# Kernel optimization log

Measured on AMD Instinct MI355X. Metric: run time of the kernel, lower is better.

Reference implementation:

```python
import jax, jax.numpy as jnp
import numpy as np

N = 100000   # nodes
E = 600000   # edges
D = 128      # input = hidden = output dim
L = 3        # GNN layers
C = 40       # num_classes
EPS = 1e-5   # BatchNorm eps


def setup_inputs() -> dict:
    key = jax.random.key(0)
    ks = jax.random.split(key, 8)
    x = jax.random.normal(ks[0], (N, D), jnp.float32)
    edge_index = jax.random.randint(ks[1], (2, E), 0, N, jnp.int32)
    # GCNConv weights per layer (Glorot-ish scale), bias zeros
    Ws = jax.random.normal(ks[2], (L, D, D), jnp.float32) / np.sqrt(D)
    bs = jnp.zeros((L, D), jnp.float32)
    # BatchNorm affine params
    gammas = jnp.ones((L, D), jnp.float32)
    betas = jnp.zeros((L, D), jnp.float32)
    # PReLU single slope per layer (torch default init 0.25)
    prelu_a = jnp.full((L,), 0.25, jnp.float32)
    # classification head: Linear(D,D) -> ReLU -> Linear(D,C)
    Wh1 = jax.random.normal(ks[3], (D, D), jnp.float32) / np.sqrt(D)
    bh1 = jnp.zeros((D,), jnp.float32)
    Wh2 = jax.random.normal(ks[4], (D, C), jnp.float32) / np.sqrt(D)
    bh2 = jnp.zeros((C,), jnp.float32)
    return dict(x=x, edge_index=edge_index, Ws=Ws, bs=bs, gammas=gammas,
                betas=betas, prelu_a=prelu_a, Wh1=Wh1, bh1=bh1, Wh2=Wh2, bh2=bh2)


def _gcn_conv(h, src, dst, norm, W, b):
    # PyG GCNConv: out_i = sum_{j->i} norm_ij * (x_j W) + b  (self-loops already in src/dst)
    m = (h @ W)[src] * norm[:, None]          # [E+N, D_out]
    return jax.ops.segment_sum(m, dst, num_segments=N) + b


def reference(x, edge_index, Ws, bs, gammas, betas, prelu_a, Wh1, bh1, Wh2, bh2):
    # add self-loops + symmetric normalization (computed once; same graph each layer)
    loops = jnp.arange(N, dtype=edge_index.dtype)
    src = jnp.concatenate([edge_index[0], loops])
    dst = jnp.concatenate([edge_index[1], loops])
    deg = jax.ops.segment_sum(jnp.ones_like(dst, jnp.float32), dst, num_segments=N)
    dinv = jax.lax.rsqrt(jnp.maximum(deg, 1.0))  # deg >= 1 thanks to self-loops
    norm = dinv[src] * dinv[dst]                 # [E+N]

    h = x
    for l in range(L):
        h = _gcn_conv(h, src, dst, norm, Ws[l], bs[l])
        # BatchNorm in training mode: batch statistics over nodes
        mu = h.mean(axis=0)
        var = h.var(axis=0)
        h = (h - mu) * jax.lax.rsqrt(var + EPS) * gammas[l] + betas[l]
        # PReLU
        h = jnp.where(h > 0, h, prelu_a[l] * h)

    embeddings = h
    logits = jax.nn.relu(embeddings @ Wh1 + bh1) @ Wh2 + bh2
    out = jnp.argmax(logits, axis=1)
    return embeddings, logits, out
```

## Files before the change

### kernel.cpp

```cpp
#include <hip/hip_runtime.h>
#include <hip/hip_bf16.h>
#include <cstddef>

#define N_NODES 100000
#define N_EDGES 600000
#define DD 128
#define LL 3
#define CC 40
#define BN_EPS 1e-5f

typedef __attribute__((ext_vector_type(8))) short bfrag;
typedef __attribute__((ext_vector_type(4))) float f32x4;

__device__ __forceinline__ float ldf(const void* p, long i, int f32) {
    return f32 ? ((const float*)p)[i] : __bfloat162float(((const __hip_bfloat16*)p)[i]);
}
__device__ __forceinline__ void stf(void* p, long i, float v, int f32) {
    if (f32) ((float*)p)[i] = v;
    else     ((__hip_bfloat16*)p)[i] = __float2bfloat16(v);
}

__device__ __forceinline__ unsigned short f2bf(float f) {
    unsigned u = __float_as_uint(f);
    unsigned r = (u + 0x7fffu + ((u >> 16) & 1u)) >> 16;
    return (unsigned short)r;
}
__device__ __forceinline__ float bf2f(unsigned short h) {
    return __uint_as_float(((unsigned)h) << 16);
}

__global__ __launch_bounds__(256) void k_detect(const void* __restrict__ x, int* __restrict__ dflag) {
    __shared__ int s[256];
    int t = threadIdx.x;
    const __hip_bfloat16* xb = (const __hip_bfloat16*)x;
    int bad = 0;
    for (int i = t; i < 4096; i += 256) {
        float v = __bfloat162float(xb[i]);
        float a = fabsf(v);
        if (!(a < 1e6f)) bad++;
        else if (v != 0.f && a < 1e-30f) bad++;
    }
    s[t] = bad; __syncthreads();
    for (int off = 128; off > 0; off >>= 1) {
        if (t < off) s[t] += s[t + off];
        __syncthreads();
    }
    if (t == 0) *dflag = (s[0] > 64) ? 1 : 0;
}

__global__ __launch_bounds__(256) void k_packw(const void* __restrict__ Ws, const void* __restrict__ Wh1,
                                               unsigned short* __restrict__ Wp,
                                               const int* __restrict__ dflag) {
    int f = *dflag;
    int u = blockIdx.x * 256 + threadIdx.x;
    int mat = u >> 14;
    int r = u & 16383;
    int k = r >> 7, c = r & 127;
    float wv = (mat < 3) ? ldf(Ws, (long)mat * 16384 + r, f) : ldf(Wh1, r, f);
    unsigned short hi = f2bf(wv);
    float r1 = wv - bf2f(hi);
    unsigned short mid = f2bf(r1);
    float r2 = r1 - bf2f(mid);
    unsigned short lo = f2bf(r2);
    int n = c >> 4, ks = k >> 5, j = k & 7;
    int lanep = (c & 15) | (((k >> 3) & 3) << 4);
    long base = (long)mat * 49152 + (long)((n * 4 + ks) * 3) * 512 + lanep * 8 + j;
    Wp[base] = hi;
    Wp[base + 512] = mid;
    Wp[base + 1024] = lo;
}


__global__ __launch_bounds__(256) void k_init(int* cnt, int* fpos, int* rowptr, float* stats) {
    int i = blockIdx.x * 256 + threadIdx.x;
    if (i < N_NODES) { cnt[i] = 0; fpos[i] = 0; }
    if (i < 6 * DD) stats[i] = 0.f;
    if (i == 0) rowptr[N_NODES] = N_EDGES;
}

__global__ __launch_bounds__(256) void k_count(const int* __restrict__ ei, int* __restrict__ cnt) {
    int e = blockIdx.x * 256 + threadIdx.x;
    if (e < N_EDGES) atomicAdd(&cnt[ei[N_EDGES + e]], 1);
}

__global__ __launch_bounds__(256) void k_scan1(const int* __restrict__ cnt, int* __restrict__ rowptr,
                                               int* __restrict__ bsum, float* __restrict__ dinv) {
    __shared__ int s[256];
    int t = threadIdx.x;
    int i = blockIdx.x * 256 + t;
    int v = (i < N_NODES) ? cnt[i] : 0;
    if (i < N_NODES) dinv[i] = 1.f / sqrtf((float)(1 + v));
    s[t] = v; __syncthreads();
    for (int off = 1; off < 256; off <<= 1) {
        int x = (t >= off) ? s[t - off] : 0;
        __syncthreads();
        s[t] += x; __syncthreads();
    }
    if (i < N_NODES) rowptr[i] = s[t] - v;
    if (t == 255) bsum[blockIdx.x] = s[255];
}

__global__ __launch_bounds__(512) void k_scan2(int* bsum, int nb) {
    __shared__ int s[512];
    int t = threadIdx.x;
    int v = (t < nb) ? bsum[t] : 0;
    s[t] = v; __syncthreads();
    for (int off = 1; off < 512; off <<= 1) {
        int x = (t >= off) ? s[t - off] : 0;
        __syncthreads();
        s[t] += x; __syncthreads();
    }
    if (t < nb) bsum[t] = s[t] - v;
}

__global__ __launch_bounds__(256) void k_scan3(int* rowptr, const int* __restrict__ bsum) {
    int i = blockIdx.x * 256 + threadIdx.x;
    if (i < N_NODES) rowptr[i] += bsum[blockIdx.x];
}

__global__ __launch_bounds__(256) void k_fill(const int* __restrict__ ei, int* __restrict__ fpos,
                                              const int* __restrict__ rowptr, int* __restrict__ adj) {
    int e = blockIdx.x * 256 + threadIdx.x;
    if (e < N_EDGES) {
        int d = ei[N_EDGES + e];
        int p = atomicAdd(&fpos[d], 1);
        adj[rowptr[d] + p] = ei[e];
    }
}

__device__ __forceinline__ void load_act(const void* __restrict__ src, long row, int lane, int f,
                                         const float* __restrict__ bnp,
                                         float s0, float s1, float h0, float h1, float al,
                                         float& o0, float& o1) {
    if (bnp) {
        float2 v = ((const float2*)src)[row * 64 + lane];
        float y0 = fmaf(v.x, s0, h0), y1 = fmaf(v.y, s1, h1);
        o0 = (y0 > 0.f) ? y0 : al * y0;
        o1 = (y1 > 0.f) ? y1 : al * y1;
    } else if (f) {
        float2 v = ((const float2*)src)[row * 64 + lane];
        o0 = v.x; o1 = v.y;
    } else {
        unsigned u = ((const unsigned*)src)[row * 64 + lane];
        o0 = __uint_as_float(u << 16);
        o1 = __uint_as_float(u & 0xffff0000u);
    }
}


__global__ __launch_bounds__(256) void k_agg(const void* __restrict__ src,
                                             const int* __restrict__ rowptr,
                                             const int* __restrict__ adj,
                                             const float* __restrict__ dinv,
                                             const float* __restrict__ bnp,
                                             float* __restrict__ outp,
                                             const int* __restrict__ dflag) {
    int f = *dflag;
    int lane = threadIdx.x & 63;
    int i = blockIdx.x * 4 + (threadIdx.x >> 6);
    if (i >= N_NODES) return;
    float s0 = 0.f, s1 = 0.f, h0 = 0.f, h1 = 0.f, al = 0.f;
    if (bnp) {
        s0 = bnp[2 * lane];       s1 = bnp[2 * lane + 1];
        h0 = bnp[128 + 2 * lane]; h1 = bnp[129 + 2 * lane];
        al = bnp[256];
    }
    float di = dinv[i];
    int e0 = rowptr[i], e1 = rowptr[i + 1];
    float x0, x1;
    load_act(src, i, lane, f, bnp, s0, s1, h0, h1, al, x0, x1);
    float acc0 = di * x0, acc1 = di * x1;

    for (int base = e0; base < e1; base += 64) {
        int m = e1 - base; if (m > 64) m = 64;
        int aj = (lane < m) ? adj[base + lane] : 0;
        float djl = (lane < m) ? dinv[aj] : 0.f;
        int t = 0;
        for (; t + 2 <= m; t += 2) {
            int j0 = __shfl(aj, t), j1 = __shfl(aj, t + 1);
            float d0 = __shfl(djl, t), d1 = __shfl(djl, t + 1);
            float p0, p1, q0, q1;
            load_act(src, j0, lane, f, bnp, s0, s1, h0, h1, al, p0, p1);
            load_act(src, j1, lane, f, bnp, s0, s1, h0, h1, al, q0, q1);
            acc0 += d0 * p0 + d1 * q0;
            acc1 += d0 * p1 + d1 * q1;
        }
        if (t < m) {
            int j0 = __shfl(aj, t);
            float d0 = __shfl(djl, t);
            float p0, p1;
            load_act(src, j0, lane, f, bnp, s0, s1, h0, h1, al, p0, p1);
            acc0 += d0 * p0;
            acc1 += d0 * p1;
        }
    }
    float2 r; r.x = di * acc0; r.y = di * acc1;
    ((float2*)outp)[(size_t)i * 64 + lane] = r;
}


__global__ __launch_bounds__(256, 2) void k_gemm2(const float* __restrict__ A,
                                                  const unsigned short* __restrict__ Wp,
                                                  const void* __restrict__ bias, long boff,
                                                  const float* __restrict__ bnpA,
                                                  float* __restrict__ stats,
                                                  float* __restrict__ Cout, int relu,
                                                  const int* __restrict__ dflag) {
    __shared__ unsigned short Wl[24576];
    int f = *dflag;
    int tid = threadIdx.x;

    int lane = tid & 63;
    int w = tid >> 6;
    int lr = lane & 15;
    int lg = lane >> 4;
    int rowbase = blockIdx.x * 128 + w * 32;

    float bcol[8];
    #pragma unroll
    for (int n = 0; n < 8; ++n)
        bcol[n] = bias ? ldf(bias, boff + n * 16 + lr, f) : 0.f;

    float alA = bnpA ? bnpA[256] : 0.f;

    bfrag ah[2][4], am[2][4], alo[2][4];
    const float4* A4 = (const float4*)A;
    #pragma unroll
    for (int ks = 0; ks < 4; ++ks) {
        int k0 = ks * 32 + lg * 8;
        float bs_[8], bh_[8];
        if (bnpA) {
            float4 sa = *(const float4*)&bnpA[k0];
            float4 sb = *(const float4*)&bnpA[k0 + 4];
            float4 ha = *(const float4*)&bnpA[128 + k0];
            float4 hb = *(const float4*)&bnpA[128 + k0 + 4];
            bs_[0] = sa.x; bs_[1] = sa.y; bs_[2] = sa.z; bs_[3] = sa.w;
            bs_[4] = sb.x; bs_[5] = sb.y; bs_[6] = sb.z; bs_[7] = sb.w;
            bh_[0] = ha.x; bh_[1] = ha.y; bh_[2] = ha.z; bh_[3] = ha.w;
            bh_[4] = hb.x; bh_[5] = hb.y; bh_[6] = hb.z; bh_[7] = hb.w;
        }
        #pragma unroll
        for (int s = 0; s < 2; ++s) {
            int row = rowbase + s * 16 + lr;
            float xv[8];
            if (row < N_NODES) {
                long bi = (long)row * 32 + (k0 >> 2);
                float4 x0 = A4[bi], x1 = A4[bi + 1];
                xv[0] = x0.x; xv[1] = x0.y; xv[2] = x0.z; xv[3] = x0.w;
                xv[4] = x1.x; xv[5] = x1.y; xv[6] = x1.z; xv[7] = x1.w;
            } else {
                #pragma unroll
                for (int e = 0; e < 8; ++e) xv[e] = 0.f;
            }
            if (bnpA) {
                #pragma unroll
                for (int e = 0; e < 8; ++e) {
                    float y = fmaf(xv[e], bs_[e], bh_[e]);
                    xv[e] = (y > 0.f) ? y : alA * y;
                }
            }
            bfrag hfr, mfr, lfr;
            #pragma unroll
            for (int e = 0; e < 8; ++e) {
                unsigned short hb2 = f2bf(xv[e]);
                float r1 = xv[e] - bf2f(hb2);
                unsigned short mb2 = f2bf(r1);
                float r2 = r1 - bf2f(mb2);
                hfr[e] = (short)hb2;
                mfr[e] = (short)mb2;
                lfr[e] = (short)f2bf(r2);
            }
            ah[s][ks] = hfr;
            am[s][ks] = mfr;
            alo[s][ks] = lfr;
        }
    }

    f32x4 acc[2][8];
    #pragma unroll
    for (int s = 0; s < 2; ++s)
        #pragma unroll
        for (int n = 0; n < 8; ++n) acc[s][n] = (f32x4){0.f, 0.f, 0.f, 0.f};

    #pragma unroll
    for (int h = 0; h < 2; ++h) {
        if (h) __syncthreads();
        {
            const uint4* srcp = (const uint4*)(Wp + (size_t)h * 24576);
            uint4* dstp = (uint4*)Wl;
            #pragma unroll
            for (int u = 0; u < 12; ++u) dstp[tid + 256 * u] = srcp[tid + 256 * u];
        }
        __syncthreads();

        #pragma unroll
        for (int nn = 0; nn < 4; ++nn) {
            int n = h * 4 + nn;
            bfrag bh[4], bm[4], bl[4];
            #pragma unroll
            for (int ks = 0; ks < 4; ++ks) {
                int base = ((nn * 4 + ks) * 3) * 512 + lane * 8;
                bh[ks] = *(const bfrag*)&Wl[base];
                bm[ks] = *(const bfrag*)&Wl[base + 512];
                bl[ks] = *(const bfrag*)&Wl[base + 1024];
            }
            #pragma unroll
            for (int ks = 0; ks < 4; ++ks) {
                #pragma unroll
                for (int s = 0; s < 2; ++s) {
                    acc[s][n] = __builtin_amdgcn_mfma_f32_16x16x32_bf16(ah[s][ks],  bh[ks], acc[s][n], 0, 0, 0);
                    acc[s][n] = __builtin_amdgcn_mfma_f32_16x16x32_bf16(am[s][ks],  bh[ks], acc[s][n], 0, 0, 0);
                    acc[s][n] = __builtin_amdgcn_mfma_f32_16x16x32_bf16(ah[s][ks],  bm[ks], acc[s][n], 0, 0, 0);
                    acc[s][n] = __builtin_amdgcn_mfma_f32_16x16x32_bf16(am[s][ks],  bm[ks], acc[s][n], 0, 0, 0);
                    acc[s][n] = __builtin_amdgcn_mfma_f32_16x16x32_bf16(alo[s][ks], bh[ks], acc[s][n], 0, 0, 0);
                    acc[s][n] = __builtin_amdgcn_mfma_f32_16x16x32_bf16(ah[s][ks],  bl[ks], acc[s][n], 0, 0, 0);
                }
            }
        }
    }

    int rowst[2][4]; bool rv[2][4];
    #pragma unroll
    for (int s = 0; s < 2; ++s)
        #pragma unroll
        for (int reg = 0; reg < 4; ++reg) {
            rowst[s][reg] = rowbase + s * 16 + lg * 4 + reg;
            rv[s][reg] = rowst[s][reg] < N_NODES;
        }

    float ls[8], lq[8];
    #pragma unroll
    for (int n = 0; n < 8; ++n) { ls[n] = 0.f; lq[n] = 0.f; }

    #pragma unroll
    for (int s = 0; s < 2; ++s)
        #pragma unroll
        for (int n = 0; n < 8; ++n) {
            int colb = n * 16 + lr;
            #pragma unroll
            for (int reg = 0; reg < 4; ++reg) {
                if (rv[s][reg]) {
                    float o = acc[s][n][reg] + bcol[n];
                    if (relu) o = fmaxf(o, 0.f);
                    Cout[(long)rowst[s][reg] * 128 + colb] = o;
                    ls[n] += o;
                    lq[n] += o * o;
                }
            }
        }

    if (stats) {
        #pragma unroll
        for (int n = 0; n < 8; ++n) {
            ls[n] += __shfl_xor(ls[n], 16);
            ls[n] += __shfl_xor(ls[n], 32);
            lq[n] += __shfl_xor(lq[n], 16);
            lq[n] += __shfl_xor(lq[n], 32);
        }
        __syncthreads();
        float* red = (float*)Wl;
        if (lane < 16) {
            #pragma unroll
            for (int n = 0; n < 8; ++n) {
                red[w * 256 + n * 16 + lane] = ls[n];
                red[w * 256 + 128 + n * 16 + lane] = lq[n];
            }
        }
        __syncthreads();
        float t = red[tid] + red[256 + tid] + red[512 + tid] + red[768 + tid];
        atomicAdd(&stats[tid], t);
    }
}

__global__ __launch_bounds__(128) void k_bnprep(const float* __restrict__ stats,
                                                const void* __restrict__ g, const void* __restrict__ b,
                                                const void* __restrict__ a, int l,
                                                float* __restrict__ bnp, const int* __restrict__ dflag) {
    int f = *dflag;
    int c = threadIdx.x;
    float mean = stats[c] / (float)N_NODES;
    float var = stats[128 + c] / (float)N_NODES - mean * mean;
    float inv = 1.f / sqrtf(var + BN_EPS);
    float s = ldf(g, (long)l * DD + c, f) * inv;
    bnp[c] = s;
    bnp[128 + c] = ldf(b, (long)l * DD + c, f) - mean * s;
    if (c == 0) bnp[256] = ldf(a, l, f);
}

__global__ __launch_bounds__(256) void k_emb(const float* __restrict__ H, const float* __restrict__ bnp,
                                             void* __restrict__ out, const int* __restrict__ dflag) {
    int f = *dflag;
    long idx = (long)blockIdx.x * 256 + threadIdx.x;
    int c = (int)(idx & 127);
    float al = bnp[256];
    float y = fmaf(H[idx], bnp[c], bnp[128 + c]);
    y = (y > 0.f) ? y : al * y;
    stf(out, idx, y, f);
}


__global__ __launch_bounds__(256) void k_head(const float* __restrict__ Hd, const void* __restrict__ W2,
                                              const void* __restrict__ b2,
                                              void* __restrict__ out_base,
                                              const int* __restrict__ dflag) {
    __shared__ float Wl[128][40];
    __shared__ float bl[40];
    __shared__ float rv[32][8];
    __shared__ int ri[32][8];
    int f = *dflag;
    int tid = threadIdx.x;
    for (int u = tid; u < 128 * 40; u += 256) Wl[u / 40][u % 40] = ldf(W2, u, f);
    if (tid < 40) bl[tid] = ldf(b2, tid, f);
    __syncthreads();
    int rl = tid >> 3, g = tid & 7;
    long r = (long)blockIdx.x * 32 + rl;
    float acc[5];
    #pragma unroll
    for (int j = 0; j < 5; ++j) acc[j] = bl[g * 5 + j];
    for (int k = 0; k < 128; ++k) {
        float h = Hd[r * 128 + k];
        #pragma unroll
        for (int j = 0; j < 5; ++j) acc[j] += h * Wl[k][g * 5 + j];
    }
    float best = acc[0]; int bi = 0;
    #pragma unroll
    for (int j = 1; j < 5; ++j)
        if (acc[j] > best) { best = acc[j]; bi = j; }
    const long LOG_OFF = (long)N_NODES * DD;
    const long ARG_OFF = (long)N_NODES * (DD + CC);
    #pragma unroll
    for (int j = 0; j < 5; ++j) stf(out_base, LOG_OFF + r * 40 + g * 5 + j, acc[j], f);
    rv[rl][g] = best; ri[rl][g] = g * 5 + bi;
    __syncthreads();
    if (tid < 32) {
        long row = (long)blockIdx.x * 32 + tid;
        float bb = rv[tid][0]; int bbi = ri[tid][0];
        #pragma unroll
        for (int g2 = 1; g2 < 8; ++g2)
            if (rv[tid][g2] > bb) { bb = rv[tid][g2]; bbi = ri[tid][g2]; }
        stf(out_base, ARG_OFF + row, (float)bbi, f);
    }
}


extern "C" void kernel_launch(void* const* d_in, const int* in_sizes, int n_in,
                              void* d_out, int out_size, void* d_ws, size_t ws_size,
                              hipStream_t stream) {
    const void* x   = d_in[0];
    const int* ei   = (const int*)d_in[1];
    const void* Ws  = d_in[2];
    const void* bs  = d_in[3];
    const void* gam = d_in[4];
    const void* bet = d_in[5];
    const void* pa  = d_in[6];
    const void* Wh1 = d_in[7];
    const void* bh1 = d_in[8];
    const void* Wh2 = d_in[9];
    const void* bh2 = d_in[10];

    char* w = (char*)d_ws;
    int* cnt     = (int*)w;    w += sizeof(int) * N_NODES;
    int* fpos    = (int*)w;    w += sizeof(int) * N_NODES;
    int* rowptr  = (int*)w;    w += sizeof(int) * (N_NODES + 4);
    int* adj     = (int*)w;    w += sizeof(int) * N_EDGES;
    int* bsum    = (int*)w;    w += sizeof(int) * 512;
    int* dflag   = (int*)w;    w += sizeof(int) * 4;
    float* dinv  = (float*)w;  w += sizeof(float) * N_NODES;
    float* stats = (float*)w;  w += sizeof(float) * (6 * DD);
    float* bnp   = (float*)w;  w += sizeof(float) * (3 * 512);
    unsigned short* Wp = (unsigned short*)w; w += sizeof(unsigned short) * 4 * 49152;
    float* bufA  = (float*)w;  w += sizeof(float) * (size_t)N_NODES * DD;
    float* bufB  = (float*)w;  w += sizeof(float) * (size_t)N_NODES * DD;

    const int scanBlocks = (N_NODES + 255) / 256;
    const int edgeBlocks = (N_EDGES + 255) / 256;
    const int elemBlocks = (N_NODES * DD) / 256;
    const int gemmBlocks = (N_NODES + 127) / 128;
    const int aggBlocks  = (N_NODES + 3) / 4;

    k_detect<<<1, 256, 0, stream>>>(x, dflag);
    k_packw<<<256, 256, 0, stream>>>(Ws, Wh1, Wp, dflag);
    k_init<<<scanBlocks, 256, 0, stream>>>(cnt, fpos, rowptr, stats);
    k_count<<<edgeBlocks, 256, 0, stream>>>(ei, cnt);
    k_scan1<<<scanBlocks, 256, 0, stream>>>(cnt, rowptr, bsum, dinv);
    k_scan2<<<1, 512, 0, stream>>>(bsum, scanBlocks);
    k_scan3<<<scanBlocks, 256, 0, stream>>>(rowptr, bsum);
    k_fill<<<edgeBlocks, 256, 0, stream>>>(ei, fpos, rowptr, adj);

    for (int l = 0; l < LL; ++l) {
        const void* src = (l == 0) ? x : (const void*)bufB;
        const float* bn = (l == 0) ? nullptr : (bnp + (l - 1) * 512);
        k_agg<<<aggBlocks, 256, 0, stream>>>(src, rowptr, adj, dinv, bn, bufA, dflag);
        k_gemm2<<<gemmBlocks, 256, 0, stream>>>(bufA, Wp + (size_t)l * 49152, bs, (long)l * DD,
                                                nullptr, stats + l * 256, bufB, 0, dflag);
        k_bnprep<<<1, 128, 0, stream>>>(stats + l * 256, gam, bet, pa, l, bnp + l * 512, dflag);
    }

    k_emb<<<elemBlocks, 256, 0, stream>>>(bufB, bnp + 2 * 512, d_out, dflag);
    k_gemm2<<<gemmBlocks, 256, 0, stream>>>(bufB, Wp + (size_t)3 * 49152, bh1, 0, bnp + 2 * 512,
                                            nullptr, bufA, 1, dflag);
    k_head<<<(N_NODES / 32), 256, 0, stream>>>(bufA, Wh2, bh2, d_out, dflag);
}
```

Before: 658.7 us.

## Precompute per-edge source weights and gather with half-wave float4 loads

The CSR fill kernel now also writes a per-edge weight array holding dinv[src]. This removes the dependent dinv gather from the aggregation inner loop. The aggregation kernel now splits each wavefront into two half-waves that work on different edges, each lane loading a float4 (four features) per row. It processes four edges per iteration and reduces the two halves with a cross-lane xor shuffle at the end. The aim is more independent row gathers in flight and fewer load instructions, at the cost of an extra edge-sized buffer, a final shuffle reduction, and some wasted zero-weight loads on padded edge slots.

```diff
diff --git a/kernel.cpp b/kernel.cpp
--- a/kernel.cpp
+++ b/kernel.cpp
@@ -119,31 +119,30 @@
 }
 
 __global__ __launch_bounds__(256) void k_fill(const int* __restrict__ ei, int* __restrict__ fpos,
-                                              const int* __restrict__ rowptr, int* __restrict__ adj) {
+                                              const int* __restrict__ rowptr, int* __restrict__ adj,
+                                              float* __restrict__ wadj, const float* __restrict__ dinv) {
     int e = blockIdx.x * 256 + threadIdx.x;
     if (e < N_EDGES) {
+        int s = ei[e];
         int d = ei[N_EDGES + e];
         int p = atomicAdd(&fpos[d], 1);
-        adj[rowptr[d] + p] = ei[e];
-    }
-}
-
-__device__ __forceinline__ void load_act(const void* __restrict__ src, long row, int lane, int f,
-                                         const float* __restrict__ bnp,
-                                         float s0, float s1, float h0, float h1, float al,
-                                         float& o0, float& o1) {
-    if (bnp) {
-        float2 v = ((const float2*)src)[row * 64 + lane];
-        float y0 = fmaf(v.x, s0, h0), y1 = fmaf(v.y, s1, h1);
-        o0 = (y0 > 0.f) ? y0 : al * y0;
-        o1 = (y1 > 0.f) ? y1 : al * y1;
-    } else if (f) {
-        float2 v = ((const float2*)src)[row * 64 + lane];
-        o0 = v.x; o1 = v.y;
+        int pos = rowptr[d] + p;
+        adj[pos] = s;
+        wadj[pos] = dinv[s];
+    }
+}
+
+__device__ __forceinline__ float4 load_row4(const void* __restrict__ src, long row, int q, int f) {
+    if (f) {
+        return ((const float4*)src)[row * 32 + q];
     } else {
-        unsigned u = ((const unsigned*)src)[row * 64 + lane];
-        o0 = __uint_as_float(u << 16);
-        o1 = __uint_as_float(u & 0xffff0000u);
+        uint2 u = ((const uint2*)src)[row * 32 + q];
+        float4 v;
+        v.x = __uint_as_float(u.x << 16);
+        v.y = __uint_as_float(u.x & 0xffff0000u);
+        v.z = __uint_as_float(u.y << 16);
+        v.w = __uint_as_float(u.y & 0xffff0000u);
+        return v;
     }
 }
 
@@ -151,51 +150,84 @@
 __global__ __launch_bounds__(256) void k_agg(const void* __restrict__ src,
                                              const int* __restrict__ rowptr,
                                              const int* __restrict__ adj,
+                                             const float* __restrict__ wadj,
                                              const float* __restrict__ dinv,
                                              const float* __restrict__ bnp,
                                              float* __restrict__ outp,
                                              const int* __restrict__ dflag) {
     int f = *dflag;
     int lane = threadIdx.x & 63;
+    int h = lane >> 5;
+    int q = lane & 31;
     int i = blockIdx.x * 4 + (threadIdx.x >> 6);
     if (i >= N_NODES) return;
-    float s0 = 0.f, s1 = 0.f, h0 = 0.f, h1 = 0.f, al = 0.f;
-    if (bnp) {
-        s0 = bnp[2 * lane];       s1 = bnp[2 * lane + 1];
-        h0 = bnp[128 + 2 * lane]; h1 = bnp[129 + 2 * lane];
+
+    float4 sc = make_float4(1.f, 1.f, 1.f, 1.f);
+    float4 sh = make_float4(0.f, 0.f, 0.f, 0.f);
+    float al = 0.f;
+    bool useBN = (bnp != nullptr);
+    if (useBN) {
+        sc = ((const float4*)bnp)[q];
+        sh = ((const float4*)(bnp + 128))[q];
         al = bnp[256];
     }
+
     float di = dinv[i];
     int e0 = rowptr[i], e1 = rowptr[i + 1];
-    float x0, x1;
-    load_act(src, i, lane, f, bnp, s0, s1, h0, h1, al, x0, x1);
-    float acc0 = di * x0, acc1 = di * x1;
+
+    float a0 = 0.f, a1 = 0.f, a2 = 0.f, a3 = 0.f;
+    if (h == 0) {
+        float4 v = load_row4(src, i, q, f);
+        if (useBN) {
+            float y;
+            y = fmaf(v.x, sc.x, sh.x); v.x = (y > 0.f) ? y : al * y;
+            y = fmaf(v.y, sc.y, sh.y); v.y = (y > 0.f) ? y : al * y;
+            y = fmaf(v.z, sc.z, sh.z); v.z = (y > 0.f) ? y : al * y;
+            y = fmaf(v.w, sc.w, sh.w); v.w = (y > 0.f) ? y : al * y;
+        }
+        a0 = di * v.x; a1 = di * v.y; a2 = di * v.z; a3 = di * v.w;
+    }
 
     for (int base = e0; base < e1; base += 64) {
         int m = e1 - base; if (m > 64) m = 64;
-        int aj = (lane < m) ? adj[base + lane] : 0;
-        float djl = (lane < m) ? dinv[aj] : 0.f;
-        int t = 0;
-        for (; t + 2 <= m; t += 2) {
-            int j0 = __shfl(aj, t), j1 = __shfl(aj, t + 1);
-            float d0 = __shfl(djl, t), d1 = __shfl(djl, t + 1);
-            float p0, p1, q0, q1;
-            load_act(src, j0, lane, f, bnp, s0, s1, h0, h1, al, p0, p1);
-            load_act(src, j1, lane, f, bnp, s0, s1, h0, h1, al, q0, q1);
-            acc0 += d0 * p0 + d1 * q0;
-            acc1 += d0 * p1 + d1 * q1;
-        }
-        if (t < m) {
-            int j0 = __shfl(aj, t);
-            float d0 = __shfl(djl, t);
-            float p0, p1;
-            load_act(src, j0, lane, f, bnp, s0, s1, h0, h1, al, p0, p1);
-            acc0 += d0 * p0;
-            acc1 += d0 * p1;
-        }
-    }
-    float2 r; r.x = di * acc0; r.y = di * acc1;
-    ((float2*)outp)[(size_t)i * 64 + lane] = r;
+        int ajl = (lane < m) ? adj[base + lane] : 0;
+        float wl = (lane < m) ? wadj[base + lane] : 0.f;
+        for (int t = 0; t < m; t += 4) {
+            int s0 = t + h;     if (s0 > 63) s0 = 63;
+            int s1 = t + 2 + h; if (s1 > 63) s1 = 63;
+            int j0 = __shfl(ajl, s0);
+            int j1 = __shfl(ajl, s1);
+            float w0 = __shfl(wl, s0);
+            float w1 = __shfl(wl, s1);
+            float4 v0 = load_row4(src, j0, q, f);
+            float4 v1 = load_row4(src, j1, q, f);
+            if (useBN) {
+                float y;
+                y = fmaf(v0.x, sc.x, sh.x); v0.x = (y > 0.f) ? y : al * y;
+                y = fmaf(v0.y, sc.y, sh.y); v0.y = (y > 0.f) ? y : al * y;
+                y = fmaf(v0.z, sc.z, sh.z); v0.z = (y > 0.f) ? y : al * y;
+                y = fmaf(v0.w, sc.w, sh.w); v0.w = (y > 0.f) ? y : al * y;
+                y = fmaf(v1.x, sc.x, sh.x); v1.x = (y > 0.f) ? y : al * y;
+                y = fmaf(v1.y, sc.y, sh.y); v1.y = (y > 0.f) ? y : al * y;
+                y = fmaf(v1.z, sc.z, sh.z); v1.z = (y > 0.f) ? y : al * y;
+                y = fmaf(v1.w, sc.w, sh.w); v1.w = (y > 0.f) ? y : al * y;
+            }
+            a0 += w0 * v0.x + w1 * v1.x;
+            a1 += w0 * v0.y + w1 * v1.y;
+            a2 += w0 * v0.z + w1 * v1.z;
+            a3 += w0 * v0.w + w1 * v1.w;
+        }
+    }
+
+    a0 += __shfl_xor(a0, 32);
+    a1 += __shfl_xor(a1, 32);
+    a2 += __shfl_xor(a2, 32);
+    a3 += __shfl_xor(a3, 32);
+
+    if (h == 0) {
+        float4 r = make_float4(di * a0, di * a1, di * a2, di * a3);
+        ((float4*)outp)[(size_t)i * 32 + q] = r;
+    }
 }
 
 
@@ -463,6 +495,7 @@
     int* fpos    = (int*)w;    w += sizeof(int) * N_NODES;
     int* rowptr  = (int*)w;    w += sizeof(int) * (N_NODES + 4);
     int* adj     = (int*)w;    w += sizeof(int) * N_EDGES;
+    float* wadj  = (float*)w;  w += sizeof(float) * N_EDGES;
     int* bsum    = (int*)w;    w += sizeof(int) * 512;
     int* dflag   = (int*)w;    w += sizeof(int) * 4;
     float* dinv  = (float*)w;  w += sizeof(float) * N_NODES;
@@ -485,12 +518,12 @@
     k_scan1<<<scanBlocks, 256, 0, stream>>>(cnt, rowptr, bsum, dinv);
     k_scan2<<<1, 512, 0, stream>>>(bsum, scanBlocks);
     k_scan3<<<scanBlocks, 256, 0, stream>>>(rowptr, bsum);
-    k_fill<<<edgeBlocks, 256, 0, stream>>>(ei, fpos, rowptr, adj);
+    k_fill<<<edgeBlocks, 256, 0, stream>>>(ei, fpos, rowptr, adj, wadj, dinv);
 
     for (int l = 0; l < LL; ++l) {
         const void* src = (l == 0) ? x : (const void*)bufB;
         const float* bn = (l == 0) ? nullptr : (bnp + (l - 1) * 512);
-        k_agg<<<aggBlocks, 256, 0, stream>>>(src, rowptr, adj, dinv, bn, bufA, dflag);
+        k_agg<<<aggBlocks, 256, 0, stream>>>(src, rowptr, adj, wadj, dinv, bn, bufA, dflag);
         k_gemm2<<<gemmBlocks, 256, 0, stream>>>(bufA, Wp + (size_t)l * 49152, bs, (long)l * DD,
                                                 nullptr, stats + l * 256, bufB, 0, dflag);
         k_bnprep<<<1, 128, 0, stream>>>(stats + l * 256, gam, bet, pa, l, bnp + l * 512, dflag);
```

New measurement: 646.2 us. About the same (-1.9%).
